# Kernel optimization log

Measured on AMD Instinct MI355X. Metric: run time of the kernel, lower is better.

## Reference

```python
import jax, jax.numpy as jnp
import numpy as np

NC = 80          # num classes (len(yolov8.names))
CONF = 0.25      # ultralytics conf_thres default
IOU_T = 0.45     # ultralytics iou_thres default
MAX_DET = 300    # module default max_det
K = 1024         # pre-NMS candidate cap (static stand-in for max_nms)
MAX_WH = 7680.0  # ultralytics class-offset for multi-class NMS


def setup_inputs() -> dict:
    key = jax.random.key(0)
    k1, k2, k3 = jax.random.split(key, 3)
    B, A = 32, 8400
    # YOLOv8 head layout: rows 0:4 = xywh (pixels), rows 4: = sigmoid class scores
    xy = jax.random.uniform(k1, (B, 2, A), dtype=jnp.float32) * 640.0
    wh = jax.random.uniform(k2, (B, 2, A), dtype=jnp.float32) * 160.0 + 8.0
    scores = jax.random.uniform(k3, (B, NC, A), dtype=jnp.float32) ** 3  # mostly below conf_thres
    preds = jnp.concatenate([xy, wh, scores], axis=1)  # [B, 4+NC, A]
    return {"preds": preds}


def _box_iou(b):
    # b: [K, 4] xyxy -> [K, K] pairwise IoU
    area = (b[:, 2] - b[:, 0]) * (b[:, 3] - b[:, 1])
    lt = jnp.maximum(b[:, None, :2], b[None, :, :2])
    rb = jnp.minimum(b[:, None, 2:], b[None, :, 2:])
    wh = jnp.clip(rb - lt, 0.0)
    inter = wh[..., 0] * wh[..., 1]
    return inter / (area[:, None] + area[None, :] - inter + 1e-7)


def _nms_single(pred):
    # pred: [4+NC, A]
    boxes_xywh = pred[:4].T           # [A, 4]
    cls_scores = pred[4:].T           # [A, NC]
    conf = cls_scores.max(-1)         # best-class confidence per anchor
    cls = jnp.argmax(cls_scores, -1)
    score = jnp.where(conf > CONF, conf, 0.0)
    top, idx = jax.lax.top_k(score, K)            # K candidates by confidence
    xywh = boxes_xywh[idx]
    half = xywh[:, 2:] * 0.5
    boxes = jnp.concatenate([xywh[:, :2] - half, xywh[:, :2] + half], -1)  # xyxy
    cls_k = cls[idx]
    valid = top > CONF
    # multi-class NMS via per-class coordinate offset (ultralytics trick)
    iou = _box_iou(boxes + (cls_k.astype(boxes.dtype) * MAX_WH)[:, None])
    ar = jnp.arange(K)

    def body(i, st):
        supp, keep = st
        ki = valid[i] & ~supp[i]
        keep = keep.at[i].set(ki)
        supp = supp | (ki & (iou[i] > IOU_T) & (ar > i))
        return supp, keep

    _, keep = jax.lax.fori_loop(0, K, body,
                                (jnp.zeros(K, bool), jnp.zeros(K, bool)))
    fscore = jnp.where(keep, top, 0.0)
    sc, order = jax.lax.top_k(fscore, MAX_DET)
    det = jnp.concatenate(
        [boxes[order], top[order][:, None], cls_k[order].astype(boxes.dtype)[:, None]], -1)
    # pad invalid rows with value NC in every column (matches F.pad(value=len(names)))
    return jnp.where((sc > CONF)[:, None], det, jnp.float32(NC))


def reference(preds):
    # [B, MAX_DET, 6] -> (x1, y1, x2, y2, conf, cls), padded rows filled with NC
    return jax.vmap(_nms_single)(preds)
```

## Files before the change

### kernel.cpp

```cpp
#include <hip/hip_runtime.h>
#include <stdint.h>

typedef unsigned long long u64;
typedef unsigned int u32;

#define NC 80
#define CONF_T 0.25f
#define IOU_THR 0.45f
#define MAX_DET 300
#define KBIG 1024
#define A_ANCH 8400
#define NROWS 84
#define MAX_WH 7680.0f
#define HBINS 256
#define BIN_BASE 0x3e80u

__device__ __forceinline__ void hadd(u32* h, u32 bin, bool m, int lane) {
    u64 act = __ballot(m);
    if (act == 0) return;
    int fl = __ffsll((unsigned long long)act) - 1;
    u32 fb = __shfl(bin, fl);
    u64 same = __ballot(m && (bin == fb));
    if (lane == fl) atomicAdd(&h[fb], (u32)__popcll(same));
    if (m && (bin != fb)) atomicAdd(&h[bin], 1u);
}

__global__ __launch_bounds__(512) void yolo_conf_kernel(const float* __restrict__ preds,
                                                        u64* __restrict__ keys,
                                                        u32* __restrict__ hist) {
    int b = blockIdx.x / 9;
    int slab = blockIdx.x % 9;
    if (slab == 0 && threadIdx.x < HBINS) hist[(size_t)b * HBINS + threadIdx.x] = 0;
    int g = slab * 512 + threadIdx.x;
    if (g >= A_ANCH / 2) return;
    int a0 = g * 2;
    const float* base = preds + ((size_t)b * NROWS + 4) * A_ANCH + a0;
    float2 best = *(const float2*)base;
    int bc0 = 0, bc1 = 0;
#pragma unroll 8
    for (int c = 1; c < NC; ++c) {
        float2 v = *(const float2*)(base + (size_t)c * A_ANCH);
        if (v.x > best.x) { best.x = v.x; bc0 = c; }
        if (v.y > best.y) { best.y = v.y; bc1 = c; }
    }
    float s0 = (best.x > CONF_T) ? best.x : 0.0f;
    float s1 = (best.y > CONF_T) ? best.y : 0.0f;
    ulonglong2 kk;
    kk.x = ((u64)__float_as_uint(s0) << 32) | ((u64)(16383 - a0) << 7) | (u64)bc0;
    kk.y = ((u64)__float_as_uint(s1) << 32) | ((u64)(16383 - (a0 + 1)) << 7) | (u64)bc1;
    *(ulonglong2*)(keys + (size_t)b * A_ANCH + a0) = kk;
}

__global__ __launch_bounds__(256) void yolo_prep_kernel(const float* __restrict__ preds,
                                                        const u64* __restrict__ keys,
                                                        float4* __restrict__ obox,
                                                        u32* __restrict__ hist) {
    __shared__ u32 lh[HBINS];
    const int lane = threadIdx.x & 63;
    int b = blockIdx.x / 33;
    int a = (blockIdx.x % 33) * 256 + threadIdx.x;
    lh[threadIdx.x] = 0;
    __syncthreads();

    u32 bits = 0, bin = 0;
    bool act = a < A_ANCH;
    if (act) {
        u64 key = keys[(size_t)b * A_ANCH + a];
        bits = (u32)(key >> 32);
        int cls = (int)(key & 127u);
        const float* pb = preds + (size_t)b * NROWS * A_ANCH + a;
        float x = pb[0];
        float y = pb[A_ANCH];
        float w = pb[2 * A_ANCH];
        float h = pb[3 * A_ANCH];
        float hw = __fmul_rn(w, 0.5f), hh = __fmul_rn(h, 0.5f);
        float x1 = __fsub_rn(x, hw), x2 = __fadd_rn(x, hw);
        float y1 = __fsub_rn(y, hh), y2 = __fadd_rn(y, hh);
        float off = __fmul_rn((float)cls, MAX_WH);
        float4 oB;
        oB.x = __fadd_rn(x1, off); oB.y = __fadd_rn(y1, off);
        oB.z = __fadd_rn(x2, off); oB.w = __fadd_rn(y2, off);
        obox[(size_t)b * A_ANCH + a] = oB;
        bin = (bits >> 16) - BIN_BASE;
        if (bin > 255u) bin = 255u;
    }
    hadd(lh, bin, act && (bits != 0u), lane);
    __syncthreads();
    u32 c = lh[threadIdx.x];
    if (c) atomicAdd(&hist[(size_t)b * HBINS + threadIdx.x], c);
}

__device__ __forceinline__ float iou_f(float ix1, float iy1, float ix2, float iy2, float iar,
                                       float jx1, float jy1, float jx2, float jy2, float jar) {
    float lx = fmaxf(ix1, jx1), ly = fmaxf(iy1, jy1);
    float rx = fminf(ix2, jx2), ry = fminf(iy2, jy2);
    float ww = fmaxf(__fsub_rn(rx, lx), 0.0f);
    float hh = fmaxf(__fsub_rn(ry, ly), 0.0f);
    float inter = __fmul_rn(ww, hh);
    float den = __fadd_rn(__fsub_rn(__fadd_rn(iar, jar), inter), 1e-7f);
    return __fdiv_rn(inter, den);
}

__device__ __forceinline__ u64 bstep(u64 v, u32 idx, u32 size, u32 stride) {
    u64 v2 = __shfl_xor((unsigned long long)v, (int)stride, 64);
    bool keep_big = (((idx & stride) == 0) == ((idx & size) == 0));
    return ((v > v2) == keep_big) ? v : v2;
}

__device__ __forceinline__ void radix_scan(u32* hist, int nb, int shift, u32* s_scal,
                                           u32* wsum, int tid, int lane, int wid) {
    int per = nb >> 9; if (per == 0) per = 1;
    int na = nb / per;
    u32 rem = s_scal[1];
    u32 Pk = s_scal[0];
    int hi = nb - 1 - per * tid;
    u32 s = 0;
    if (tid < na)
        for (int q = 0; q < per; ++q) s += hist[hi - q];
    u32 pre = s;
#pragma unroll
    for (int off = 1; off < 64; off <<= 1) {
        u32 o = __shfl_up(pre, off);
        if (lane >= off) pre += o;
    }
    if (lane == 63) wsum[wid] = pre;
    __syncthreads();
    u32 base = 0;
    for (int w = 0; w < wid; ++w) base += wsum[w];
    u32 run = base + pre - s;
    if (tid < na) {
        for (int q = 0; q < per; ++q) {
            int d = hi - q;
            u32 g = hist[d];
            if (run < rem && rem <= run + g) {
                s_scal[0] = Pk | ((u32)d << shift);
                s_scal[1] = rem - run;
            }
            run += g;
        }
    }
    __syncthreads();
}

union U2 {
    u32 hist[4096];
    struct { u32 eqw[264]; u32 wpre[264]; } tie;
};

__global__ __launch_bounds__(512) void yolo_nms_kernel(const float* __restrict__ preds,
                                                       const u64* __restrict__ keys,
                                                       const float4* __restrict__ obox,
                                                       const u32* __restrict__ hist,
                                                       float* __restrict__ out) {
    const int b = blockIdx.x;
    const int tid = threadIdx.x;
    const int lane = tid & 63;
    const int wid = tid >> 6;

    __shared__ U2 u2;
    __shared__ u64 skey[KBIG];
    __shared__ float BX1[KBIG], BY1[KBIG], BX2[KBIG], BY2[KBIG], BAR[KBIG];
    __shared__ int keptlist[364];
    __shared__ float kx1[364], ky1[364], kx2[364], ky2[364], kar[364];
    __shared__ u32 kcls[364];
    __shared__ u64 rows[64];
    __shared__ u32 wsum[8];
    __shared__ u32 s_scal[4];
    __shared__ u32 s_cnt;
    __shared__ u32 s_csupp[2];
    __shared__ u32 s_nkept;

    const u64* kb = keys + (size_t)b * A_ANCH;
    const u32* hb = hist + (size_t)b * HBINS;

    u32 hg = (tid < HBINS) ? hb[HBINS - 1 - tid] : 0u;

    u32 vals[17];
#pragma unroll
    for (int it = 0; it < 17; ++it) {
        int a = tid + it * 512;
        vals[it] = (a < A_ANCH) ? (u32)(kb[a] >> 32) : 0u;
    }

    {
        u32 pre = hg;
#pragma unroll
        for (int off = 1; off < 64; off <<= 1) {
            u32 o = __shfl_up(pre, off);
            if (lane >= off) pre += o;
        }
        if (lane == 63) wsum[wid] = pre;
        __syncthreads();
        u32 base = 0;
        for (int w = 0; w < wid; ++w) base += wsum[w];
        pre += base;
        u32 run = pre - hg;
        if (tid < HBINS) {
            if (run < 512u && 512u <= pre) { s_scal[0] = (u32)(HBINS - 1 - tid); s_scal[2] = pre; }
            if (tid == HBINS - 1) {
                s_scal[3] = pre;
                if (pre < 512u) { s_scal[0] = 0; s_scal[2] = pre; }
            }
        }
        __syncthreads();
    }
    const u32 Pbin16 = BIN_BASE + s_scal[0];
    const u32 Cfast = s_scal[2];
    const u32 validN = s_scal[3];

    for (int pass = 0; pass < 2; ++pass) {
        u32 Ccand;
        if (pass == 0) {
            if (Cfast > (u32)KBIG) continue;
            Ccand = Cfast;
            skey[tid] = 0; skey[tid + 512] = 0;
            if (tid == 0) { s_cnt = 0; s_nkept = 0; s_csupp[0] = 0; s_csupp[1] = 0; }
            __syncthreads();
#pragma unroll
            for (int it = 0; it < 17; ++it) {
                int a = tid + it * 512;
                u32 v = vals[it];
                bool take = (a < A_ANCH) && (v != 0u) && ((v >> 16) >= Pbin16);
                u64 m = __ballot(take);
                if (m) {
                    int fl = __ffsll((unsigned long long)m) - 1;
                    u32 basep = 0;
                    if (lane == fl) basep = atomicAdd(&s_cnt, (u32)__popcll(m));
                    basep = __shfl(basep, fl);
                    if (take) {
                        u32 pos = basep + (u32)__popcll(m & ((1ull << lane) - 1ull));
                        if (pos < (u32)KBIG) skey[pos] = kb[a];
                    }
                }
            }
            __syncthreads();
        } else {
            for (int i = tid; i < 4096; i += 512) u2.hist[i] = 0;
            if (tid == 0) {
                s_scal[0] = 0; s_scal[1] = (u32)KBIG; s_scal[2] = 0;
                s_nkept = 0; s_csupp[0] = 0; s_csupp[1] = 0;
            }
            __syncthreads();
#pragma unroll
            for (int it = 0; it < 17; ++it) {
                int a = tid + it * 512;
                hadd(u2.hist, vals[it] >> 20, a < A_ANCH, lane);
            }
            __syncthreads();
            radix_scan(u2.hist, 4096, 20, s_scal, wsum, tid, lane, wid);
            for (int i = tid; i < 4096; i += 512) u2.hist[i] = 0;
            __syncthreads();
            u32 Pk = s_scal[0];
#pragma unroll
            for (int it = 0; it < 17; ++it) {
                int a = tid + it * 512;
                u32 v = vals[it];
                bool m = (a < A_ANCH) && ((v & 0xFFF00000u) == Pk);
                hadd(u2.hist, (v >> 8) & 4095u, m, lane);
            }
            __syncthreads();
            radix_scan(u2.hist, 4096, 8, s_scal, wsum, tid, lane, wid);
            for (int i = tid; i < 256; i += 512) u2.hist[i] = 0;
            __syncthreads();
            Pk = s_scal[0];
#pragma unroll
            for (int it = 0; it < 17; ++it) {
                int a = tid + it * 512;
                u32 v = vals[it];
                bool m = (a < A_ANCH) && ((v & 0xFFFFFF00u) == Pk);
                hadd(u2.hist, v & 255u, m, lane);
            }
            __syncthreads();
            radix_scan(u2.hist, 256, 0, s_scal, wsum, tid, lane, wid);
            const u32 P = s_scal[0];
            const u32 tEq = s_scal[1];
            if (tid < 264) u2.tie.eqw[tid] = 0;
            __syncthreads();
#pragma unroll
            for (int it = 0; it < 17; ++it) {
                int a = tid + it * 512;
                if (a < A_ANCH && vals[it] == P) atomicOr(&u2.tie.eqw[a >> 5], 1u << (a & 31));
            }
            __syncthreads();
            if (wid == 0) {
                u32 cw[5], loc = 0;
#pragma unroll
                for (int q = 0; q < 5; ++q) {
                    int w2 = lane * 5 + q;
                    u32 e = (w2 < 264) ? u2.tie.eqw[w2] : 0u;
                    cw[q] = (u32)__popc(e); loc += cw[q];
                }
                u32 pre = loc;
#pragma unroll
                for (int off = 1; off < 64; off <<= 1) {
                    u32 o = __shfl_up(pre, off);
                    if (lane >= off) pre += o;
                }
                u32 run = pre - loc;
#pragma unroll
                for (int q = 0; q < 5; ++q) {
                    int w2 = lane * 5 + q;
                    if (w2 < 264) u2.tie.wpre[w2] = run;
                    run += cw[q];
                }
            }
            __syncthreads();
#pragma unroll
            for (int it = 0; it < 17; ++it) {
                int a = tid + it * 512;
                bool take = false;
                if (a < A_ANCH) {
                    u32 v = vals[it];
                    take = v > P;
                    if (!take && v == P) {
                        u32 r = u2.tie.wpre[a >> 5] +
                                (u32)__popc(u2.tie.eqw[a >> 5] & ((1u << (a & 31)) - 1u));
                        take = (r < tEq);
                    }
                }
                u64 m = __ballot(take);
                if (m) {
                    int fl = __ffsll((unsigned long long)m) - 1;
                    u32 basep = 0;
                    if (lane == fl) basep = atomicAdd(&s_scal[2], (u32)__popcll(m));
                    basep = __shfl(basep, fl);
                    if (take) {
                        u32 pos = basep + (u32)__popcll(m & ((1ull << lane) - 1ull));
                        if (pos < (u32)KBIG) skey[pos] = kb[a];
                    }
                }
            }
            __syncthreads();
            Ccand = KBIG;
        }

        {
            u64 vA = skey[tid], vB = skey[tid + 512];
            const u32 iA = (u32)tid, iB = (u32)tid + 512;
#pragma unroll
            for (u32 size = 2; size <= 64; size <<= 1)
#pragma unroll
                for (u32 stride = size >> 1; stride >= 1; stride >>= 1) {
                    vA = bstep(vA, iA, size, stride);
                    vB = bstep(vB, iB, size, stride);
                }
            skey[tid] = vA; skey[tid + 512] = vB;
            __syncthreads();
            for (u32 size = 128; size <= 1024; size <<= 1) {
                for (u32 stride = size >> 1; stride >= 64; stride >>= 1) {
                    u32 i1 = ((tid & ~(int)(stride - 1)) << 1) | (tid & (stride - 1));
                    u32 i2 = i1 + stride;
                    bool desc = ((i1 & size) == 0);
                    u64 x = skey[i1], y = skey[i2];
                    if ((x < y) == desc) { skey[i1] = y; skey[i2] = x; }
                    __syncthreads();
                }
                vA = skey[tid]; vB = skey[tid + 512];
#pragma unroll
                for (u32 stride = 32; stride >= 1; stride >>= 1) {
                    vA = bstep(vA, iA, size, stride);
                    vB = bstep(vB, iB, size, stride);
                }
                skey[tid] = vA; skey[tid + 512] = vB;
                __syncthreads();
            }
        }

#pragma unroll
        for (int q = 0; q < 2; ++q) {
            int t = tid + q * 512;
            u64 key = skey[t];
            int idx = 16383 - (int)((key >> 7) & 16383u);
            if (idx >= A_ANCH || idx < 0) idx = 0;
            float4 ob = obox[(size_t)b * A_ANCH + idx];
            BX1[t] = ob.x; BY1[t] = ob.y; BX2[t] = ob.z; BY2[t] = ob.w;
            BAR[t] = __fmul_rn(__fsub_rn(ob.z, ob.x), __fsub_rn(ob.w, ob.y));
        }
        __syncthreads();

        const int nchunks = (int)((Ccand + 63u) >> 6);
        for (int c = 0; c < nchunks; ++c) {
            int j = c * 64 + lane;
            u64 keyj = skey[j];
            float scj = __uint_as_float((u32)(keyj >> 32));
            u32 clsj = (u32)(keyj & 127u);
            float jx1 = BX1[j], jy1 = BY1[j], jx2 = BX2[j], jy2 = BY2[j], jar = BAR[j];

            u32 nk = s_nkept;
            bool suppbit = false;
            for (u32 k = wid; k < nk; k += 8) {
                bool cm = (kcls[k] == clsj);
                if (__ballot(cm)) {
                    float iou = iou_f(kx1[k], ky1[k], kx2[k], ky2[k], kar[k],
                                      jx1, jy1, jx2, jy2, jar);
                    suppbit |= (cm && (iou > IOU_THR));
                }
            }
            u64 bm = __ballot(suppbit);
            if (bm && lane == 0) {
                atomicOr(&s_csupp[0], (u32)bm);
                atomicOr(&s_csupp[1], (u32)(bm >> 32));
            }

#pragma unroll
            for (int p2 = 0; p2 < 8; ++p2) {
                int i = p2 * 8 + wid;
                int ci = c * 64 + i;
                u32 clsi = (u32)(skey[ci] & 127u);
                u64 m = 0;
                if (__ballot(clsi == clsj)) {
                    float iou = iou_f(BX1[ci], BY1[ci], BX2[ci], BY2[ci], BAR[ci],
                                      jx1, jy1, jx2, jy2, jar);
                    m = __ballot((lane > i) && (iou > IOU_THR));
                }
                if (lane == 0) rows[i] = m;
            }
            __syncthreads();

            if (wid == 0) {
                u64 row = rows[lane];
                u32 rlo = (u32)row, rhi = (u32)(row >> 32);
                u64 csupp = (((u64)s_csupp[1]) << 32) | (u64)s_csupp[0];
                u64 validm = __ballot(scj > CONF_T) & ~csupp;
                u64 supp = 0, keep = 0;
#pragma unroll
                for (int i = 0; i < 64; ++i) {
                    u64 ri = (((u64)(u32)__builtin_amdgcn_readlane((int)rhi, i)) << 32) |
                             (u64)(u32)__builtin_amdgcn_readlane((int)rlo, i);
                    bool ki = (((validm & ~supp) >> i) & 1ull) != 0;
                    if (ki) { keep |= (1ull << i); supp |= ri; }
                }
                u32 basek = s_nkept;
                if ((keep >> lane) & 1ull) {
                    u32 slot = basek + (u32)__popcll(keep & ((1ull << lane) - 1ull));
                    keptlist[slot] = j;
                    kx1[slot] = jx1; ky1[slot] = jy1;
                    kx2[slot] = jx2; ky2[slot] = jy2;
                    kar[slot] = jar; kcls[slot] = clsj;
                }
                if (lane == 0) {
                    s_nkept = basek + (u32)__popcll(keep);
                    s_csupp[0] = 0; s_csupp[1] = 0;
                }
            }
            __syncthreads();
            if (s_nkept >= MAX_DET) break;
        }

        u32 nk = s_nkept;
        bool finished = (nk >= MAX_DET) || (Ccand >= validN) || (pass == 1);
        if (!finished) continue;

        if (tid < MAX_DET) {
            float row[6];
            int t = (tid < (int)(nk < MAX_DET ? nk : MAX_DET)) ? keptlist[tid] : -1;
            if (t >= 0) {
                u64 key = skey[t];
                float score = __uint_as_float((u32)(key >> 32));
                int cls = (int)(key & 127u);
                int idx = 16383 - (int)((key >> 7) & 16383u);
                if (idx >= A_ANCH || idx < 0) idx = 0;
                const float* pb = preds + (size_t)b * NROWS * A_ANCH + idx;
                float x = pb[0], y = pb[A_ANCH], w = pb[2 * A_ANCH], h = pb[3 * A_ANCH];
                float hw = __fmul_rn(w, 0.5f), hh = __fmul_rn(h, 0.5f);
                row[0] = __fsub_rn(x, hw);
                row[1] = __fsub_rn(y, hh);
                row[2] = __fadd_rn(x, hw);
                row[3] = __fadd_rn(y, hh);
                row[4] = score;
                row[5] = (float)cls;
            } else {
                row[0] = row[1] = row[2] = row[3] = row[4] = row[5] = (float)NC;
            }
            float* o = out + ((size_t)b * MAX_DET + tid) * 6;
#pragma unroll
            for (int q = 0; q < 6; ++q) o[q] = row[q];
        }
        break;
    }
}

extern "C" void kernel_launch(void* const* d_in, const int* in_sizes, int n_in,
                              void* d_out, int out_size, void* d_ws, size_t ws_size,
                              hipStream_t stream) {
    const float* preds = (const float*)d_in[0];
    float* out = (float*)d_out;
    int B = in_sizes[0] / (NROWS * A_ANCH);
    u64* keys = (u64*)d_ws;
    float4* obox = (float4*)(keys + (size_t)B * A_ANCH);
    u32* hist = (u32*)(obox + (size_t)B * A_ANCH);
    yolo_conf_kernel<<<dim3(B * 9), dim3(512), 0, stream>>>(preds, keys, hist);
    yolo_prep_kernel<<<dim3(B * 33), dim3(256), 0, stream>>>(preds, keys, obox, hist);
    yolo_nms_kernel<<<dim3(B), dim3(512), 0, stream>>>(preds, keys, obox, hist, out);
}
```

Before: 73.59 us.

## Split NMS into select-sort, parallel IoU-matrix, and bitmask-reduction kernels with fallback

Splits the single per-image NMS kernel into a fast path of three kernels: select and bitonic-sort the top candidates, build the full 512x512 IoU suppression bitmask with 8 blocks per image, then run a 64-wide greedy reduction over those bitmasks. The point is to spread the IoU work over many more blocks instead of one block per image doing everything serially. Images the fast path cannot finish (too many candidates, or under MAX_DET kept among the first 512 while more valid boxes remain) are marked not done and handled by the original kernel, now a fallback that exits early for finished images. The cost is three more launches, extra global-memory round trips for sorted keys and row masks, and a fallback launch that still runs even when every image is done.

```diff
diff --git a/kernel.cpp b/kernel.cpp
--- a/kernel.cpp
+++ b/kernel.cpp
@@ -61,7 +61,6 @@
     int a = (blockIdx.x % 33) * 256 + threadIdx.x;
     lh[threadIdx.x] = 0;
     __syncthreads();
-
     u32 bits = 0, bin = 0;
     bool act = a < A_ANCH;
     if (act) {
@@ -142,17 +141,259 @@
     __syncthreads();
 }
 
+__global__ __launch_bounds__(512) void yolo_selsort_kernel(const u64* __restrict__ keys,
+                                                           const u32* __restrict__ hist,
+                                                           u64* __restrict__ sortk,
+                                                           u32* __restrict__ meta) {
+    const int b = blockIdx.x;
+    const int tid = threadIdx.x;
+    const int lane = tid & 63;
+    const int wid = tid >> 6;
+
+    __shared__ u64 skey[KBIG];
+    __shared__ u32 wsum[8];
+    __shared__ u32 s_scal[4];
+    __shared__ u32 s_cnt;
+
+    const u64* kb = keys + (size_t)b * A_ANCH;
+    const u32* hb = hist + (size_t)b * HBINS;
+
+    u32 hg = (tid < HBINS) ? hb[HBINS - 1 - tid] : 0u;
+    u32 vals[17];
+#pragma unroll
+    for (int it = 0; it < 17; ++it) {
+        int a = tid + it * 512;
+        vals[it] = (a < A_ANCH) ? (u32)(kb[a] >> 32) : 0u;
+    }
+    {
+        u32 pre = hg;
+#pragma unroll
+        for (int off = 1; off < 64; off <<= 1) {
+            u32 o = __shfl_up(pre, off);
+            if (lane >= off) pre += o;
+        }
+        if (lane == 63) wsum[wid] = pre;
+        __syncthreads();
+        u32 base = 0;
+        for (int w = 0; w < wid; ++w) base += wsum[w];
+        pre += base;
+        u32 run = pre - hg;
+        if (tid < HBINS) {
+            if (run < 512u && 512u <= pre) { s_scal[0] = (u32)(HBINS - 1 - tid); s_scal[2] = pre; }
+            if (tid == HBINS - 1) {
+                s_scal[3] = pre;
+                if (pre < 512u) { s_scal[0] = 0; s_scal[2] = pre; }
+            }
+        }
+        __syncthreads();
+    }
+    const u32 Pbin16 = BIN_BASE + s_scal[0];
+    const u32 Cfast = s_scal[2];
+    const u32 validN = s_scal[3];
+    if (tid == 0) { meta[b * 2] = Cfast; meta[b * 2 + 1] = validN; }
+    if (Cfast > (u32)KBIG) return;
+
+    skey[tid] = 0; skey[tid + 512] = 0;
+    if (tid == 0) s_cnt = 0;
+    __syncthreads();
+#pragma unroll
+    for (int it = 0; it < 17; ++it) {
+        int a = tid + it * 512;
+        u32 v = vals[it];
+        bool take = (a < A_ANCH) && (v != 0u) && ((v >> 16) >= Pbin16);
+        u64 m = __ballot(take);
+        if (m) {
+            int fl = __ffsll((unsigned long long)m) - 1;
+            u32 basep = 0;
+            if (lane == fl) basep = atomicAdd(&s_cnt, (u32)__popcll(m));
+            basep = __shfl(basep, fl);
+            if (take) {
+                u32 pos = basep + (u32)__popcll(m & ((1ull << lane) - 1ull));
+                if (pos < (u32)KBIG) skey[pos] = kb[a];
+            }
+        }
+    }
+    __syncthreads();
+
+    {
+        u64 vA = skey[tid], vB = skey[tid + 512];
+        const u32 iA = (u32)tid, iB = (u32)tid + 512;
+#pragma unroll
+        for (u32 size = 2; size <= 64; size <<= 1)
+#pragma unroll
+            for (u32 stride = size >> 1; stride >= 1; stride >>= 1) {
+                vA = bstep(vA, iA, size, stride);
+                vB = bstep(vB, iB, size, stride);
+            }
+        skey[tid] = vA; skey[tid + 512] = vB;
+        __syncthreads();
+        for (u32 size = 128; size <= 1024; size <<= 1) {
+            for (u32 stride = size >> 1; stride >= 64; stride >>= 1) {
+                u32 i1 = ((tid & ~(int)(stride - 1)) << 1) | (tid & (stride - 1));
+                u32 i2 = i1 + stride;
+                bool desc = ((i1 & size) == 0);
+                u64 x = skey[i1], y = skey[i2];
+                if ((x < y) == desc) { skey[i1] = y; skey[i2] = x; }
+                __syncthreads();
+            }
+            vA = skey[tid]; vB = skey[tid + 512];
+#pragma unroll
+            for (u32 stride = 32; stride >= 1; stride >>= 1) {
+                vA = bstep(vA, iA, size, stride);
+                vB = bstep(vB, iB, size, stride);
+            }
+            skey[tid] = vA; skey[tid + 512] = vB;
+            __syncthreads();
+        }
+    }
+    u64* so = sortk + (size_t)b * KBIG;
+    so[tid] = skey[tid];
+    so[tid + 512] = skey[tid + 512];
+}
+
+__global__ __launch_bounds__(512) void yolo_mat_kernel(const u64* __restrict__ sortk,
+                                                       const float4* __restrict__ obox,
+                                                       u64* __restrict__ rows) {
+    const int b = blockIdx.x >> 3;
+    const int m = blockIdx.x & 7;
+    const int tid = threadIdx.x;
+    const int lane = tid & 63;
+    const int wid = tid >> 6;
+    __shared__ float bx1[512], by1[512], bx2[512], by2[512], bar[512];
+
+    const u64* sk = sortk + (size_t)b * KBIG;
+    {
+        u64 key = sk[tid];
+        int idx = 16383 - (int)((key >> 7) & 16383u);
+        if (idx >= A_ANCH || idx < 0) idx = 0;
+        float4 ob = obox[(size_t)b * A_ANCH + idx];
+        bx1[tid] = ob.x; by1[tid] = ob.y; bx2[tid] = ob.z; by2[tid] = ob.w;
+        bar[tid] = __fmul_rn(__fsub_rn(ob.z, ob.x), __fsub_rn(ob.w, ob.y));
+    }
+    __syncthreads();
+
+#pragma unroll
+    for (int rr = 0; rr < 8; ++rr) {
+        int i = m * 64 + wid * 8 + rr;
+        float ix1 = bx1[i], iy1 = by1[i], ix2 = bx2[i], iy2 = by2[i], iar = bar[i];
+        u64* rowp = rows + ((size_t)b * 512 + i) * 8;
+#pragma unroll
+        for (int wd = 0; wd < 8; ++wd) {
+            int j = wd * 64 + lane;
+            float iou = iou_f(ix1, iy1, ix2, iy2, iar, bx1[j], by1[j], bx2[j], by2[j], bar[j]);
+            u64 mbit = __ballot((j > i) && (iou > IOU_THR));
+            if (lane == 0) rowp[wd] = mbit;
+        }
+    }
+}
+
+__global__ __launch_bounds__(512) void yolo_rec_kernel(const float* __restrict__ preds,
+                                                       const u64* __restrict__ sortk,
+                                                       const u64* __restrict__ rows,
+                                                       const u32* __restrict__ meta,
+                                                       u32* __restrict__ done,
+                                                       float* __restrict__ out) {
+    const int b = blockIdx.x;
+    const int tid = threadIdx.x;
+    const int lane = tid & 63;
+    const int wid = tid >> 6;
+    __shared__ u64 skl[512];
+    __shared__ u64 supp[8];
+    __shared__ u64 s_keep;
+    __shared__ int keptlist[364];
+    __shared__ u32 s_nkept;
+
+    const u32 Cfast = meta[b * 2];
+    const u32 validN = meta[b * 2 + 1];
+    skl[tid] = sortk[(size_t)b * KBIG + tid];
+    if (tid < 8) supp[tid] = 0;
+    if (tid == 0) s_nkept = 0;
+    __syncthreads();
+
+    bool ok = (Cfast <= (u32)KBIG);
+    if (ok) {
+        const u64* rb = rows + (size_t)b * 512 * 8;
+        for (int c = 0; c < 8; ++c) {
+            if (wid == 0) {
+                int i = c * 64 + lane;
+                u64 key = skl[i];
+                float sc = __uint_as_float((u32)(key >> 32));
+                u64 ri = rb[(size_t)i * 8 + c];
+                u64 validm = __ballot(sc > CONF_T) & ~supp[c];
+                u32 rlo = (u32)ri, rhi = (u32)(ri >> 32);
+                u64 sup = 0, keep = 0;
+#pragma unroll
+                for (int i2 = 0; i2 < 64; ++i2) {
+                    u64 rr = (((u64)(u32)__builtin_amdgcn_readlane((int)rhi, i2)) << 32) |
+                             (u64)(u32)__builtin_amdgcn_readlane((int)rlo, i2);
+                    bool ki = (((validm & ~sup) >> i2) & 1ull) != 0;
+                    if (ki) { keep |= (1ull << i2); sup |= rr; }
+                }
+                u32 basek = s_nkept;
+                if ((keep >> lane) & 1ull) {
+                    u32 slot = basek + (u32)__popcll(keep & ((1ull << lane) - 1ull));
+                    keptlist[slot] = i;
+                }
+                if (lane == 0) { s_keep = keep; s_nkept = basek + (u32)__popcll(keep); }
+            }
+            __syncthreads();
+            {
+                u64 k = s_keep;
+                u64 t = ((k >> lane) & 1ull) ? rb[(size_t)(c * 64 + lane) * 8 + wid] : 0ull;
+#pragma unroll
+                for (int off = 32; off >= 1; off >>= 1)
+                    t |= (u64)__shfl_xor((unsigned long long)t, off, 64);
+                if (lane == 0) supp[wid] |= t;
+            }
+            __syncthreads();
+            if (s_nkept >= MAX_DET) break;
+        }
+    }
+    u32 nk = ok ? s_nkept : 0;
+    bool fin = ok && ((nk >= MAX_DET) || (validN <= 512u));
+    if (tid == 0) done[b] = fin ? 1u : 0u;
+    if (!fin) return;
+
+    if (tid < MAX_DET) {
+        float row[6];
+        int t = (tid < (int)(nk < MAX_DET ? nk : MAX_DET)) ? keptlist[tid] : -1;
+        if (t >= 0) {
+            u64 key = skl[t];
+            float score = __uint_as_float((u32)(key >> 32));
+            int cls = (int)(key & 127u);
+            int idx = 16383 - (int)((key >> 7) & 16383u);
+            if (idx >= A_ANCH || idx < 0) idx = 0;
+            const float* pb = preds + (size_t)b * NROWS * A_ANCH + idx;
+            float x = pb[0], y = pb[A_ANCH], w = pb[2 * A_ANCH], h = pb[3 * A_ANCH];
+            float hw = __fmul_rn(w, 0.5f), hh = __fmul_rn(h, 0.5f);
+            row[0] = __fsub_rn(x, hw);
+            row[1] = __fsub_rn(y, hh);
+            row[2] = __fadd_rn(x, hw);
+            row[3] = __fadd_rn(y, hh);
+            row[4] = score;
+            row[5] = (float)cls;
+        } else {
+            row[0] = row[1] = row[2] = row[3] = row[4] = row[5] = (float)NC;
+        }
+        float* o = out + ((size_t)b * MAX_DET + tid) * 6;
+#pragma unroll
+        for (int q = 0; q < 6; ++q) o[q] = row[q];
+    }
+}
+
 union U2 {
     u32 hist[4096];
     struct { u32 eqw[264]; u32 wpre[264]; } tie;
 };
 
-__global__ __launch_bounds__(512) void yolo_nms_kernel(const float* __restrict__ preds,
-                                                       const u64* __restrict__ keys,
-                                                       const float4* __restrict__ obox,
-                                                       const u32* __restrict__ hist,
-                                                       float* __restrict__ out) {
+__global__ __launch_bounds__(512) void yolo_fallback_kernel(const float* __restrict__ preds,
+                                                            const u64* __restrict__ keys,
+                                                            const float4* __restrict__ obox,
+                                                            const u32* __restrict__ hist,
+                                                            const u32* __restrict__ done,
+                                                            float* __restrict__ out) {
     const int b = blockIdx.x;
+    if (done[b]) return;
     const int tid = threadIdx.x;
     const int lane = tid & 63;
     const int wid = tid >> 6;
@@ -172,16 +413,13 @@
 
     const u64* kb = keys + (size_t)b * A_ANCH;
     const u32* hb = hist + (size_t)b * HBINS;
-
     u32 hg = (tid < HBINS) ? hb[HBINS - 1 - tid] : 0u;
-
     u32 vals[17];
 #pragma unroll
     for (int it = 0; it < 17; ++it) {
         int a = tid + it * 512;
         vals[it] = (a < A_ANCH) ? (u32)(kb[a] >> 32) : 0u;
     }
-
     {
         u32 pre = hg;
 #pragma unroll
@@ -401,7 +639,6 @@
                 atomicOr(&s_csupp[0], (u32)bm);
                 atomicOr(&s_csupp[1], (u32)(bm >> 32));
             }
-
 #pragma unroll
             for (int p2 = 0; p2 < 8; ++p2) {
                 int i = p2 * 8 + wid;
@@ -416,7 +653,6 @@
                 if (lane == 0) rows[i] = m;
             }
             __syncthreads();
-
             if (wid == 0) {
                 u64 row = rows[lane];
                 u32 rlo = (u32)row, rhi = (u32)(row >> 32);
@@ -486,10 +722,17 @@
     const float* preds = (const float*)d_in[0];
     float* out = (float*)d_out;
     int B = in_sizes[0] / (NROWS * A_ANCH);
-    u64* keys = (u64*)d_ws;
-    float4* obox = (float4*)(keys + (size_t)B * A_ANCH);
-    u32* hist = (u32*)(obox + (size_t)B * A_ANCH);
+    float4* obox = (float4*)d_ws;
+    u64* keys = (u64*)(obox + (size_t)B * A_ANCH);
+    u64* sortk = keys + (size_t)B * A_ANCH;
+    u64* rows = sortk + (size_t)B * KBIG;
+    u32* hist = (u32*)(rows + (size_t)B * 512 * 8);
+    u32* meta = hist + (size_t)B * HBINS;
+    u32* done = meta + (size_t)B * 2;
     yolo_conf_kernel<<<dim3(B * 9), dim3(512), 0, stream>>>(preds, keys, hist);
     yolo_prep_kernel<<<dim3(B * 33), dim3(256), 0, stream>>>(preds, keys, obox, hist);
-    yolo_nms_kernel<<<dim3(B), dim3(512), 0, stream>>>(preds, keys, obox, hist, out);
-}
+    yolo_selsort_kernel<<<dim3(B), dim3(512), 0, stream>>>(keys, hist, sortk, meta);
+    yolo_mat_kernel<<<dim3(B * 8), dim3(512), 0, stream>>>(sortk, obox, rows);
+    yolo_rec_kernel<<<dim3(B), dim3(512), 0, stream>>>(preds, sortk, rows, meta, done, out);
+    yolo_fallback_kernel<<<dim3(B), dim3(512), 0, stream>>>(preds, keys, obox, hist, done, out);
+}
```

New measurement: 65.86 us. 10.5% less time.
